# Kernel tuning notes

Measured on AMD Instinct MI355X. Metric: run time of the kernel, lower is better.

## Reference

```python
import jax, jax.numpy as jnp
import numpy as np
import math

NUM_EMBED = 1024
EMBED_FEATS = 256
IN_FEATS = 512
COMMITMENT_COST = 0.25
B, T = 16, 4096


def setup_inputs() -> dict:
    key = jax.random.key(0)
    k1, k2, k3, k4 = jax.random.split(key, 4)
    inputs = jax.random.normal(k1, (B, IN_FEATS, T), dtype=jnp.float32)
    # Conv1d(kernel_size=1) == per-position linear: weight [E, C_in], bias [E]
    proj_w = jax.random.normal(k2, (EMBED_FEATS, IN_FEATS), dtype=jnp.float32) / np.sqrt(IN_FEATS)
    proj_b = jax.random.normal(k3, (EMBED_FEATS,), dtype=jnp.float32) * 0.01
    embed = jax.random.normal(k4, (NUM_EMBED, EMBED_FEATS), dtype=jnp.float32)
    return {"inputs": inputs, "proj_w": proj_w, "proj_b": proj_b, "embed": embed}


def reference(inputs, proj_w, proj_b, embed):
    sg = jax.lax.stop_gradient
    b, c_in, t = inputs.shape
    # 1x1 conv projection then transpose(1,-1): [B, T, E]
    x = jnp.einsum('bct,ec->bte', inputs, proj_w) + proj_b
    flat = x.reshape(-1, EMBED_FEATS)  # [B*T, E]
    d2 = (jnp.sum(flat * flat, axis=1, keepdims=True)
          + jnp.sum(embed * embed, axis=1)
          - 2.0 * flat @ embed.T)  # [B*T, num_embed]
    q_idx = jnp.argmin(d2, axis=1)  # [B*T]
    # one-hot @ embed == direct gather (same math, same gradient structure)
    z_q = embed[q_idx].reshape(x.shape)  # [B, T, E]
    vq_loss = jnp.mean((z_q - sg(x)) ** 2)
    commitment_loss = jnp.mean((sg(z_q) - x) ** 2)
    loss = vq_loss + COMMITMENT_COST * commitment_loss
    z_q_st = x + sg(z_q - x)  # straight-through
    n_tokens = flat.shape[0]
    probs = jnp.zeros((NUM_EMBED,), dtype=jnp.float32).at[q_idx].add(1.0) / n_tokens
    log_perplexity = -jnp.sum(probs * jnp.log(probs + 1e-10))
    num_spatial = n_tokens / b
    kldiv_r = math.log(NUM_EMBED) * num_spatial * jnp.ones((b, 1), dtype=jnp.float32)
    z_q_out = jnp.swapaxes(z_q_st, 1, 2)  # [B, E, T]
    return z_q_out, loss, kldiv_r, log_perplexity
```

## Files before the change

kernel.cpp:

```cpp
#include <hip/hip_runtime.h>
#include <hip/hip_bf16.h>
#include <math.h>

#define TT   4096
#define BB   16
#define NTOK 65536
#define CIN  512
#define EF   256
#define NE   1024

typedef __attribute__((ext_vector_type(8))) short bf16x8;
typedef __attribute__((ext_vector_type(4))) float f32x4;

static __device__ __forceinline__ unsigned short f2bf(float f) {
  unsigned int u = __float_as_uint(f);
  u += 0x7fffu + ((u >> 16) & 1u);
  return (unsigned short)(u >> 16);
}

#define GLL(gsrc, ldst) \
  __builtin_amdgcn_global_load_lds((const __attribute__((address_space(1))) void*)(gsrc), \
                                   (__attribute__((address_space(3))) void*)(ldst), 16, 0, 0)

__global__ __launch_bounds__(256) void k_prep(const float* __restrict__ Wf,
                                              const float* __restrict__ Ef,
                                              unsigned short* __restrict__ Wbf,
                                              unsigned short* __restrict__ Ebf,
                                              float* __restrict__ e_norm) {
  int bid = blockIdx.x;
  if (bid < 512) {
    int i = bid * 256 + threadIdx.x;
    Wbf[i] = f2bf(Wf[i]);
  } else if (bid < 1536) {
    int i = (bid - 512) * 256 + threadIdx.x;
    Ebf[i] = f2bf(-2.0f * Ef[i]);
  } else {
    int w = threadIdx.x >> 6, l = threadIdx.x & 63;
    int k = (bid - 1536) * 4 + w;
    const float4 v4 = ((const float4*)(Ef + (size_t)k * EF))[l];
    float s = v4.x * v4.x + v4.y * v4.y + v4.z * v4.z + v4.w * v4.w;
    for (int off = 32; off; off >>= 1) s += __shfl_down(s, off);
    if (l == 0) e_norm[k] = s;
  }
}

__global__ __launch_bounds__(256, 2) void k_fused(const float* __restrict__ in,
                                                  const unsigned short* __restrict__ Wbf,
                                                  const float* __restrict__ bias,
                                                  const unsigned short* __restrict__ Ebf,
                                                  const float* __restrict__ e_norm,
                                                  int* __restrict__ bi_out,
                                                  unsigned int* __restrict__ hist,
                                                  float* __restrict__ sse) {
  __shared__ unsigned short lds[32768];
  unsigned short* as_ = lds;
  unsigned short* bs = lds + 4096;
  unsigned short* xs = lds;
  unsigned short* es = lds + 16384;

  int tid = threadIdx.x;
  int w = tid >> 6, l = tid & 63;
  int l15 = l & 15, quad = l >> 4;
  int tok0 = blockIdx.x * 64;
  int bidx = tok0 >> 12;
  int tg0 = tok0 & 4095;
  const float* src = in + (size_t)bidx * CIN * TT + tg0;

  f32x4 acc[4][4];
#pragma unroll
  for (int a = 0; a < 4; ++a)
#pragma unroll
    for (int b = 0; b < 4; ++b) acc[a][b] = (f32x4){0.f, 0.f, 0.f, 0.f};

  for (int ks = 0; ks < 8; ++ks) {
    int k0 = ks * 64;
    float v[16];
    const float* s0 = src + (size_t)(k0 + w * 16) * TT + l;
#pragma unroll
    for (int i = 0; i < 16; ++i) v[i] = s0[(size_t)i * TT];
#pragma unroll
    for (int i = 0; i < 8; ++i) {
      int g = i * 256 + tid;
      int row = g >> 3, pc = g & 7, lc = pc ^ (row & 7);
      GLL(Wbf + (size_t)row * CIN + k0 + lc * 8, bs + g * 8);
    }
#pragma unroll
    for (int cc = 0; cc < 2; ++cc) {
      alignas(16) unsigned short tmp[8];
#pragma unroll
      for (int j = 0; j < 8; ++j) tmp[j] = f2bf(v[cc * 8 + j]);
      int c8 = w * 2 + cc;
      int pc = c8 ^ (l & 7);
      *(bf16x8*)(as_ + l * 64 + pc * 8) = *(const bf16x8*)tmp;
    }
    __syncthreads();
#pragma unroll
    for (int s = 0; s < 2; ++s) {
      int lcb = s * 4 + quad;
      bf16x8 af[4], bfr[4];
#pragma unroll
      for (int msub = 0; msub < 4; ++msub) {
        int row = msub * 16 + l15;
        int pc = lcb ^ (row & 7);
        af[msub] = *(const bf16x8*)(as_ + row * 64 + pc * 8);
      }
#pragma unroll
      for (int nsub = 0; nsub < 4; ++nsub) {
        int row = w * 64 + nsub * 16 + l15;
        int pc = lcb ^ (row & 7);
        bfr[nsub] = *(const bf16x8*)(bs + row * 64 + pc * 8);
      }
#pragma unroll
      for (int msub = 0; msub < 4; ++msub)
#pragma unroll
        for (int nsub = 0; nsub < 4; ++nsub)
          acc[msub][nsub] = __builtin_amdgcn_mfma_f32_16x16x32_bf16(af[msub], bfr[nsub],
                                                                    acc[msub][nsub], 0, 0, 0);
    }
    __syncthreads();
  }

  float xsq = 0.f;
  float bv4[4];
#pragma unroll
  for (int nsub = 0; nsub < 4; ++nsub) bv4[nsub] = bias[w * 64 + nsub * 16 + l15];
#pragma unroll
  for (int msub = 0; msub < 4; ++msub)
#pragma unroll
    for (int nsub = 0; nsub < 4; ++nsub)
#pragma unroll
      for (int reg = 0; reg < 4; ++reg) {
        int m = msub * 16 + quad * 4 + reg;
        int e = w * 64 + nsub * 16 + l15;
        float x = acc[msub][nsub][reg] + bv4[nsub];
        xsq += x * x;
        int cx = e >> 3, pcx = cx ^ (m & 31);
        xs[m * 256 + pcx * 8 + (e & 7)] = f2bf(x);
      }
  __syncthreads();

  float best_v[4][4];
  int best_i[4][4];
#pragma unroll
  for (int a = 0; a < 4; ++a)
#pragma unroll
    for (int b = 0; b < 4; ++b) { best_v[a][b] = 3.0e38f; best_i[a][b] = 0; }

  for (int chunk = 0; chunk < 4; ++chunk) {
    int c0 = chunk * 256;
    f32x4 dacc[4][4];
#pragma unroll
    for (int nsub = 0; nsub < 4; ++nsub) {
      float en = e_norm[c0 + w * 64 + nsub * 16 + l15];
#pragma unroll
      for (int msub = 0; msub < 4; ++msub) dacc[msub][nsub] = (f32x4){en, en, en, en};
    }
    for (int ks = 0; ks < 4; ++ks) {
      int k0 = ks * 64;
#pragma unroll
      for (int i = 0; i < 8; ++i) {
        int g = i * 256 + tid;
        int row = g >> 3, pc = g & 7, lc = pc ^ (row & 7);
        GLL(Ebf + (size_t)(c0 + row) * EF + k0 + lc * 8, es + g * 8);
      }
      __syncthreads();
#pragma unroll
      for (int s = 0; s < 2; ++s) {
        bf16x8 af[4], bfr[4];
        int cx = ks * 8 + s * 4 + quad;
#pragma unroll
        for (int msub = 0; msub < 4; ++msub) {
          int row = msub * 16 + l15;
          int pcx = cx ^ (row & 31);
          af[msub] = *(const bf16x8*)(xs + row * 256 + pcx * 8);
        }
        int ck = s * 4 + quad;
#pragma unroll
        for (int nsub = 0; nsub < 4; ++nsub) {
          int row = w * 64 + nsub * 16 + l15;
          int pc = ck ^ (row & 7);
          bfr[nsub] = *(const bf16x8*)(es + row * 64 + pc * 8);
        }
#pragma unroll
        for (int msub = 0; msub < 4; ++msub)
#pragma unroll
          for (int nsub = 0; nsub < 4; ++nsub)
            dacc[msub][nsub] = __builtin_amdgcn_mfma_f32_16x16x32_bf16(af[msub], bfr[nsub],
                                                                       dacc[msub][nsub], 0, 0, 0);
      }
      __syncthreads();
    }
#pragma unroll
    for (int msub = 0; msub < 4; ++msub)
#pragma unroll
      for (int nsub = 0; nsub < 4; ++nsub) {
        int code = c0 + w * 64 + nsub * 16 + l15;
#pragma unroll
        for (int reg = 0; reg < 4; ++reg) {
          float v = dacc[msub][nsub][reg];
          if (v < best_v[msub][reg]) { best_v[msub][reg] = v; best_i[msub][reg] = code; }
        }
      }
  }

#pragma unroll
  for (int msub = 0; msub < 4; ++msub)
#pragma unroll
    for (int reg = 0; reg < 4; ++reg) {
      float v = best_v[msub][reg];
      int idx = best_i[msub][reg];
#pragma unroll
      for (int off = 8; off; off >>= 1) {
        float ov = __shfl_xor(v, off, 16);
        int oi = __shfl_xor(idx, off, 16);
        if (ov < v || (ov == v && oi < idx)) { v = ov; idx = oi; }
      }
      best_v[msub][reg] = v;
      best_i[msub][reg] = idx;
    }
  float* red_v = (float*)es;
  int* red_i = (int*)(es) + 256;
  float* xred = (float*)(es) + 512;
  if (l15 == 0) {
#pragma unroll
    for (int msub = 0; msub < 4; ++msub)
#pragma unroll
      for (int reg = 0; reg < 4; ++reg) {
        int m = msub * 16 + quad * 4 + reg;
        red_v[w * 64 + m] = best_v[msub][reg];
        red_i[w * 64 + m] = best_i[msub][reg];
      }
  }
  for (int off = 32; off; off >>= 1) xsq += __shfl_down(xsq, off);
  if (l == 0) xred[w] = xsq;
  __syncthreads();
  if (tid < 64) {
    float v = red_v[tid];
    int idx = red_i[tid];
#pragma unroll
    for (int wj = 1; wj < 4; ++wj) {
      float ov = red_v[wj * 64 + tid];
      int oi = red_i[wj * 64 + tid];
      if (ov < v || (ov == v && oi < idx)) { v = ov; idx = oi; }
    }
    bi_out[tok0 + tid] = idx;
    atomicAdd(&hist[idx], 1u);
    float sv = v;
    for (int off = 32; off; off >>= 1) sv += __shfl_down(sv, off);
    if (tid == 0) atomicAdd(sse, sv + xred[0] + xred[1] + xred[2] + xred[3]);
  }
}

__global__ __launch_bounds__(256) void k_gather(const float* __restrict__ embed,
                                                const int* __restrict__ bi,
                                                float* __restrict__ out) {
  __shared__ float zq[EF * 32];
  __shared__ int idxs[32];
  int tid = threadIdx.x;
  int tok0 = blockIdx.x * 32;
  if (tid < 32) idxs[tid] = bi[tok0 + tid];
  __syncthreads();
  int w = tid >> 6, l = tid & 63;
  for (int r = 0; r < 8; ++r) {
    int tl = r * 4 + w;
    const float* erow = embed + (size_t)idxs[tl] * EF;
#pragma unroll
    for (int jj = 0; jj < 4; ++jj) {
      int e = l + 64 * jj;
      zq[e * 32 + ((tl + e) & 31)] = erow[e];
    }
  }
  __syncthreads();
  int b = tok0 >> 12;
  int t0 = tok0 & 4095;
  int tloc = l & 31;
  for (int rr = 0; rr < 32; ++rr) {
    int e = rr * 8 + w * 2 + (l >> 5);
    out[((size_t)(b * EF + e) << 12) + t0 + tloc] = zq[e * 32 + ((tloc + e) & 31)];
  }
}

__global__ __launch_bounds__(256) void k_final(const unsigned int* __restrict__ hist,
                                               const float* __restrict__ sse,
                                               float* __restrict__ out) {
  __shared__ float red[4];
  int tid = threadIdx.x;
  float local = 0.f;
  for (int i = tid; i < NE; i += 256) {
    float p = (float)hist[i] * (1.0f / 65536.0f);
    local -= p * logf(p + 1e-10f);
  }
  for (int off = 32; off; off >>= 1) local += __shfl_down(local, off);
  if ((tid & 63) == 0) red[tid >> 6] = local;
  __syncthreads();
  if (tid == 0) {
    float lp = red[0] + red[1] + red[2] + red[3];
    out[16777216] = 1.25f * sse[0] / 16777216.0f;
    out[16777233] = lp;
  }
  if (tid < 16) out[16777217 + tid] = 6.93147180559945f * 4096.0f;
}

extern "C" void kernel_launch(void* const* d_in, const int* in_sizes, int n_in,
                              void* d_out, int out_size, void* d_ws, size_t ws_size,
                              hipStream_t stream) {
  const float* inputs = (const float*)d_in[0];
  const float* proj_w = (const float*)d_in[1];
  const float* proj_b = (const float*)d_in[2];
  const float* embed = (const float*)d_in[3];
  float* out = (float*)d_out;
  char* ws = (char*)d_ws;

  unsigned short* Wbf  = (unsigned short*)(ws);
  unsigned short* Ebf  = (unsigned short*)(ws + 262144);
  float* e_norm        = (float*)(ws + 786432);
  int* bi              = (int*)(ws + 790528);
  unsigned int* hist   = (unsigned int*)(ws + 1052672);
  float* sse           = (float*)(ws + 1056768);
  if (ws_size < 1056772) return;

  hipMemsetAsync(ws + 1052672, 0, 4100, stream);

  k_prep<<<1792, 256, 0, stream>>>(proj_w, embed, Wbf, Ebf, e_norm);
  k_fused<<<1024, 256, 0, stream>>>(inputs, Wbf, proj_b, Ebf, e_norm, bi, hist, sse);
  k_gather<<<2048, 256, 0, stream>>>(embed, bi, out);
  k_final<<<1, 256, 0, stream>>>(hist, sse, out);
}
```

Before: 316.7 us.

## Shrink fused kernel LDS and registers, retile gather with vectorized stores

The fused kernel now streams the codebook in 128-code chunks instead of 256, which cuts the distance accumulators in half and reduces shared memory from 64KB to 48KB. It also splits the input loads into two halves of 8 to lower peak register pressure and reorders the bias epilogue. The aim is higher occupancy, traded for more chunk iterations and more barriers. The gather kernel is retiled to 128 tokens by 64 features per block, with float4 global loads, float4 coalesced stores and a padded shared-memory transpose.

```diff
diff --git a/kernel.cpp b/kernel.cpp
--- a/kernel.cpp
+++ b/kernel.cpp
@@ -52,7 +52,7 @@
                                                   int* __restrict__ bi_out,
                                                   unsigned int* __restrict__ hist,
                                                   float* __restrict__ sse) {
-  __shared__ unsigned short lds[32768];
+  __shared__ unsigned short lds[24576];
   unsigned short* as_ = lds;
   unsigned short* bs = lds + 4096;
   unsigned short* xs = lds;
@@ -74,10 +74,6 @@
 
   for (int ks = 0; ks < 8; ++ks) {
     int k0 = ks * 64;
-    float v[16];
-    const float* s0 = src + (size_t)(k0 + w * 16) * TT + l;
-#pragma unroll
-    for (int i = 0; i < 16; ++i) v[i] = s0[(size_t)i * TT];
 #pragma unroll
     for (int i = 0; i < 8; ++i) {
       int g = i * 256 + tid;
@@ -86,9 +82,13 @@
     }
 #pragma unroll
     for (int cc = 0; cc < 2; ++cc) {
+      float v[8];
+      const float* s0 = src + (size_t)(k0 + w * 16 + cc * 8) * TT + l;
+#pragma unroll
+      for (int i = 0; i < 8; ++i) v[i] = s0[(size_t)i * TT];
       alignas(16) unsigned short tmp[8];
 #pragma unroll
-      for (int j = 0; j < 8; ++j) tmp[j] = f2bf(v[cc * 8 + j]);
+      for (int j = 0; j < 8; ++j) tmp[j] = f2bf(v[j]);
       int c8 = w * 2 + cc;
       int pc = c8 ^ (l & 7);
       *(bf16x8*)(as_ + l * 64 + pc * 8) = *(const bf16x8*)tmp;
@@ -121,22 +121,22 @@
   }
 
   float xsq = 0.f;
-  float bv4[4];
-#pragma unroll
-  for (int nsub = 0; nsub < 4; ++nsub) bv4[nsub] = bias[w * 64 + nsub * 16 + l15];
-#pragma unroll
-  for (int msub = 0; msub < 4; ++msub)
-#pragma unroll
-    for (int nsub = 0; nsub < 4; ++nsub)
+#pragma unroll
+  for (int nsub = 0; nsub < 4; ++nsub) {
+    float bv = bias[w * 64 + nsub * 16 + l15];
+    int e = w * 64 + nsub * 16 + l15;
+    int cx = e >> 3;
+#pragma unroll
+    for (int msub = 0; msub < 4; ++msub)
 #pragma unroll
       for (int reg = 0; reg < 4; ++reg) {
         int m = msub * 16 + quad * 4 + reg;
-        int e = w * 64 + nsub * 16 + l15;
-        float x = acc[msub][nsub][reg] + bv4[nsub];
+        float x = acc[msub][nsub][reg] + bv;
         xsq += x * x;
-        int cx = e >> 3, pcx = cx ^ (m & 31);
+        int pcx = cx ^ (m & 31);
         xs[m * 256 + pcx * 8 + (e & 7)] = f2bf(x);
       }
+  }
   __syncthreads();
 
   float best_v[4][4];
@@ -146,19 +146,19 @@
 #pragma unroll
     for (int b = 0; b < 4; ++b) { best_v[a][b] = 3.0e38f; best_i[a][b] = 0; }
 
-  for (int chunk = 0; chunk < 4; ++chunk) {
-    int c0 = chunk * 256;
-    f32x4 dacc[4][4];
-#pragma unroll
-    for (int nsub = 0; nsub < 4; ++nsub) {
-      float en = e_norm[c0 + w * 64 + nsub * 16 + l15];
+  for (int chunk = 0; chunk < 8; ++chunk) {
+    int c0 = chunk * 128;
+    f32x4 dacc[4][2];
+#pragma unroll
+    for (int nsub = 0; nsub < 2; ++nsub) {
+      float en = e_norm[c0 + w * 32 + nsub * 16 + l15];
 #pragma unroll
       for (int msub = 0; msub < 4; ++msub) dacc[msub][nsub] = (f32x4){en, en, en, en};
     }
     for (int ks = 0; ks < 4; ++ks) {
       int k0 = ks * 64;
 #pragma unroll
-      for (int i = 0; i < 8; ++i) {
+      for (int i = 0; i < 4; ++i) {
         int g = i * 256 + tid;
         int row = g >> 3, pc = g & 7, lc = pc ^ (row & 7);
         GLL(Ebf + (size_t)(c0 + row) * EF + k0 + lc * 8, es + g * 8);
@@ -166,7 +166,7 @@
       __syncthreads();
 #pragma unroll
       for (int s = 0; s < 2; ++s) {
-        bf16x8 af[4], bfr[4];
+        bf16x8 af[4], bfr[2];
         int cx = ks * 8 + s * 4 + quad;
 #pragma unroll
         for (int msub = 0; msub < 4; ++msub) {
@@ -176,15 +176,15 @@
         }
         int ck = s * 4 + quad;
 #pragma unroll
-        for (int nsub = 0; nsub < 4; ++nsub) {
-          int row = w * 64 + nsub * 16 + l15;
+        for (int nsub = 0; nsub < 2; ++nsub) {
+          int row = w * 32 + nsub * 16 + l15;
           int pc = ck ^ (row & 7);
           bfr[nsub] = *(const bf16x8*)(es + row * 64 + pc * 8);
         }
 #pragma unroll
         for (int msub = 0; msub < 4; ++msub)
 #pragma unroll
-          for (int nsub = 0; nsub < 4; ++nsub)
+          for (int nsub = 0; nsub < 2; ++nsub)
             dacc[msub][nsub] = __builtin_amdgcn_mfma_f32_16x16x32_bf16(af[msub], bfr[nsub],
                                                                        dacc[msub][nsub], 0, 0, 0);
       }
@@ -193,8 +193,8 @@
 #pragma unroll
     for (int msub = 0; msub < 4; ++msub)
 #pragma unroll
-      for (int nsub = 0; nsub < 4; ++nsub) {
-        int code = c0 + w * 64 + nsub * 16 + l15;
+      for (int nsub = 0; nsub < 2; ++nsub) {
+        int code = c0 + w * 32 + nsub * 16 + l15;
 #pragma unroll
         for (int reg = 0; reg < 4; ++reg) {
           float v = dacc[msub][nsub][reg];
@@ -254,29 +254,31 @@
 __global__ __launch_bounds__(256) void k_gather(const float* __restrict__ embed,
                                                 const int* __restrict__ bi,
                                                 float* __restrict__ out) {
-  __shared__ float zq[EF * 32];
-  __shared__ int idxs[32];
+  __shared__ float zq[128 * 65];
+  __shared__ int idxs[128];
   int tid = threadIdx.x;
-  int tok0 = blockIdx.x * 32;
-  if (tid < 32) idxs[tid] = bi[tok0 + tid];
-  __syncthreads();
-  int w = tid >> 6, l = tid & 63;
+  int tok0 = blockIdx.x * 128;
+  int e0 = blockIdx.y * 64;
+  if (tid < 128) idxs[tid] = bi[tok0 + tid];
+  __syncthreads();
+  int l15 = tid & 15, tg = tid >> 4;
   for (int r = 0; r < 8; ++r) {
-    int tl = r * 4 + w;
-    const float* erow = embed + (size_t)idxs[tl] * EF;
-#pragma unroll
-    for (int jj = 0; jj < 4; ++jj) {
-      int e = l + 64 * jj;
-      zq[e * 32 + ((tl + e) & 31)] = erow[e];
-    }
-  }
-  __syncthreads();
-  int b = tok0 >> 12;
-  int t0 = tok0 & 4095;
-  int tloc = l & 31;
-  for (int rr = 0; rr < 32; ++rr) {
-    int e = rr * 8 + w * 2 + (l >> 5);
-    out[((size_t)(b * EF + e) << 12) + t0 + tloc] = zq[e * 32 + ((tloc + e) & 31)];
+    int tl = r * 16 + tg;
+    const float4 v = *(const float4*)(embed + (size_t)idxs[tl] * EF + e0 + l15 * 4);
+    float* zr = zq + tl * 65 + l15 * 4;
+    zr[0] = v.x; zr[1] = v.y; zr[2] = v.z; zr[3] = v.w;
+  }
+  __syncthreads();
+  int b = tok0 >> 12, t0 = tok0 & 4095;
+  int tl4 = (tid & 31) * 4;
+  for (int r = 0; r < 8; ++r) {
+    int e = r * 8 + (tid >> 5);
+    float4 v;
+    v.x = zq[(tl4 + 0) * 65 + e];
+    v.y = zq[(tl4 + 1) * 65 + e];
+    v.z = zq[(tl4 + 2) * 65 + e];
+    v.w = zq[(tl4 + 3) * 65 + e];
+    *(float4*)(out + ((size_t)(b * EF + e0 + e) << 12) + t0 + tl4) = v;
   }
 }
 
@@ -323,6 +325,6 @@
 
   k_prep<<<1792, 256, 0, stream>>>(proj_w, embed, Wbf, Ebf, e_norm);
   k_fused<<<1024, 256, 0, stream>>>(inputs, Wbf, proj_b, Ebf, e_norm, bi, hist, sse);
-  k_gather<<<2048, 256, 0, stream>>>(embed, bi, out);
+  k_gather<<<dim3(512, 4), 256, 0, stream>>>(embed, bi, out);
   k_final<<<1, 256, 0, stream>>>(hist, sse, out);
 }
```

New measurement: 333.2 us. +5.2%, slower.
